# Optimization experiments

Hardware: AMD Instinct MI355X
Metric: run time of the kernel (lower is better)

The kernel has to match this reference:

```python
import jax, jax.numpy as jnp
import numpy as np

K, N, M, P, H = 8, 16, 8, 32, 32
BSZ, T = 128, 512
TAU = 0.5
P_STAY = 0.9


def setup_inputs() -> dict:
    key = jax.random.key(0)
    ks = jax.random.split(key, 20)
    f32 = jnp.float32
    norm = lambda k, s, sc=1.0: (jax.random.normal(k, s) * sc).astype(f32)
    sw = 1.0 / np.sqrt(H)  # torch GRU init scale
    return {
        "a_seq": norm(ks[0], (BSZ, T, P)),
        "A": norm(ks[1], (K, N, N), 0.1),
        "Bmat": norm(ks[2], (K, N, M), 0.1),
        "C": norm(ks[3], (K, P, N), 0.1),
        "Q": (jnp.tile(jnp.eye(N, dtype=f32)[None], (K, 1, 1)) + norm(ks[4], (K, N, N), 0.01)),
        "wih_f": norm(ks[5], (3 * H, P), sw),
        "whh_f": norm(ks[6], (3 * H, H), sw),
        "bih_f": norm(ks[7], (3 * H,), sw),
        "bhh_f": norm(ks[8], (3 * H,), sw),
        "wih_b": norm(ks[9], (3 * H, P), sw),
        "whh_b": norm(ks[10], (3 * H, H), sw),
        "bih_b": norm(ks[11], (3 * H,), sw),
        "bhh_b": norm(ks[12], (3 * H,), sw),
        "wl": norm(ks[13], (K * K, 2 * H), sw),
        "bl": norm(ks[14], (K * K,), sw),
        "wi": norm(ks[15], (K, 2 * H), sw),
        "bi": norm(ks[16], (K,), sw),
        "u0": jax.random.uniform(ks[17], (BSZ, K), minval=1e-6, maxval=1.0 - 1e-6, dtype=f32),
        "useq": jax.random.uniform(ks[18], (BSZ, T - 1, K), minval=1e-6, maxval=1.0 - 1e-6, dtype=f32),
    }


def _gru_dir(gx, whh, bhh, reverse):
    # gx: [T, B, 3H] precomputed input-to-hidden gates; torch GRU cell math
    def step(h, g):
        gh = h @ whh.T + bhh
        xr, xz, xn = jnp.split(g, 3, axis=-1)
        hr, hz, hn = jnp.split(gh, 3, axis=-1)
        r = jax.nn.sigmoid(xr + hr)
        z = jax.nn.sigmoid(xz + hz)
        n = jnp.tanh(xn + r * hn)
        h_new = (1.0 - z) * n + z * h
        return h_new, h_new
    h0 = jnp.zeros((gx.shape[1], whh.shape[1]), gx.dtype)
    _, hs = jax.lax.scan(step, h0, gx, reverse=reverse)
    return hs  # [T, B, H]


def reference(a_seq, A, Bmat, C, Q, wih_f, whh_f, bih_f, bhh_f,
              wih_b, whh_b, bih_b, bhh_b, wl, bl, wi, bi, u0, useq):
    Bn, Tn, _ = a_seq.shape
    Kn = A.shape[0]
    x = a_seq.transpose(1, 0, 2)  # [T, B, P]
    hf = _gru_dir(x @ wih_f.T + bih_f, whh_f, bhh_f, False)
    hb = _gru_dir(x @ wih_b.T + bih_b, whh_b, bhh_b, True)
    h_seq = jnp.concatenate([hf, hb], axis=-1)  # [T, B, 2H]

    logits = (h_seq @ wl.T + bl).reshape(Tn, Bn, Kn, Kn)  # [T, B, K, K]
    init_logits = h_seq[0] @ wi.T + bi                     # [B, K]

    g0 = -jnp.log(-jnp.log(u0))
    gseq = -jnp.log(-jnp.log(useq))  # [B, T-1, K]

    # t = 0 (soft gumbel-softmax since is_training=True)
    y0 = jax.nn.softmax((init_logits + g0) / TAU, axis=-1)
    lq0 = (y0 * jax.nn.log_softmax(init_logits, axis=-1)).sum(-1)
    lp0 = (y0 * jnp.log(1.0 / Kn)).sum(-1)  # torch: full_like(1/K).log()

    trans = jnp.full((Kn, Kn), (1.0 - P_STAY) / (Kn - 1), a_seq.dtype)
    trans = trans.at[jnp.arange(Kn), jnp.arange(Kn)].set(P_STAY)

    def step(y_prev, xs):
        lg, g = xs  # lg: [B, K, K], g: [B, K]
        l_t = jnp.einsum('bk,bkj->bj', y_prev, lg)
        y_t = jax.nn.softmax((l_t + g) / TAU, axis=-1)
        lq = (y_t * jax.nn.log_softmax(l_t, axis=-1)).sum(-1)
        tp = y_prev @ trans
        lp = (y_t * jnp.log(jnp.clip(tp, 1e-8))).sum(-1)
        return y_t, (y_t, lq, lp)

    _, (ys, lqs, lps) = jax.lax.scan(step, y0, (logits[1:], gseq.transpose(1, 0, 2)))

    y_seq = jnp.concatenate([y0[None], ys], axis=0).transpose(1, 0, 2)  # [B, T, K]
    log_qseq = jnp.concatenate([lq0[None], lqs], axis=0).T              # [B, T]
    log_pseq = jnp.concatenate([lp0[None], lps], axis=0).T              # [B, T]

    A_seq = jnp.einsum('btk,kij->btij', y_seq, A)
    B_seq = jnp.einsum('btk,knm->btnm', y_seq, Bmat)
    Q_seq = jnp.einsum('btk,kij->btij', y_seq, Q)
    C_seq = jnp.broadcast_to(C[0], (Bn, Tn) + C[0].shape)
    return (A_seq, B_seq, C_seq, Q_seq, log_qseq, log_pseq)
```

## Files before the change

kernel.cpp:

```cpp
#include <hip/hip_runtime.h>
#include <math.h>

#define T 512
#define B 128
#define KK 8
#define HH 32
#define PP 32

#define WS_GX    0
#define WS_GS    6291456
#define WS_HSEQ  12582912
#define WS_LOGITS 0
#define WS_INIT  16777216
#define WS_YSEQ  16778240

#define OUT_A    0
#define OUT_B    16777216
#define OUT_C    25165824
#define OUT_Q    58720256
#define OUT_LQ   75497472
#define OUT_LP   75563008

#define TINV 2.0f
#define PSTAY 0.9f
#define OFFV (0.1f / 7.0f)
#define DPS (PSTAY - OFFV)
#define LOG_INV_K (-2.0794415416798357f)

typedef float f4v __attribute__((ext_vector_type(4)));
typedef __attribute__((address_space(3))) float as3f;

__device__ __forceinline__ void dma16(unsigned ldsbyte, int voffbyte, const void* sbase) {
    asm volatile("s_mov_b32 m0, %0\n\t"
                 "global_load_lds_dwordx4 %1, %2"
                 :: "s"(ldsbyte), "v"(voffbyte), "s"(sbase)
                 : "memory");
}
__device__ __forceinline__ void st16(void* p, f4v v) {
    asm volatile("global_store_dwordx4 %0, %1, off" :: "v"(p), "v"(v) : "memory");
}
__device__ __forceinline__ f4v ldsr16(int addr) {
    f4v out;
    asm volatile("ds_read_b128 %0, %1" : "=v"(out) : "v"(addr));
    return out;
}
__device__ __forceinline__ f4v ldg16(const void* p) {
    f4v out;
    asm volatile("global_load_dwordx4 %0, %1, off" : "=v"(out) : "v"(p) : "memory");
    return out;
}
__device__ __forceinline__ float ldg4(const void* p) {
    float out;
    asm volatile("global_load_dword %0, %1, off" : "=v"(out) : "v"(p) : "memory");
    return out;
}

__global__ __launch_bounds__(192) void gx_kernel(
    const float* __restrict__ a_seq,
    const float* __restrict__ wih_f, const float* __restrict__ bih_f,
    const float* __restrict__ wih_b, const float* __restrict__ bih_b,
    float* __restrict__ gx) {
    __shared__ float xt[64 * 32];
    int blk = blockIdx.x;
    int b = blk >> 3;
    int t0 = (blk & 7) << 6;
    int g = threadIdx.x;
    int dir = (g >= 96) ? 1 : 0;
    int gg = dir ? (g - 96) : g;
    const float* w = dir ? wih_b : wih_f;
    const float* bv = dir ? bih_b : bih_f;

    {
        const float4* src = (const float4*)(a_seq + ((size_t)b * T + t0) * PP);
        float4* dst = (float4*)xt;
        for (int idx = g; idx < 512; idx += 192) dst[idx] = src[idx];
    }
    float wreg[32];
#pragma unroll
    for (int q = 0; q < 8; ++q) {
        float4 wv = *(const float4*)(w + (size_t)gg * PP + q * 4);
        wreg[q * 4 + 0] = wv.x; wreg[q * 4 + 1] = wv.y;
        wreg[q * 4 + 2] = wv.z; wreg[q * 4 + 3] = wv.w;
    }
    float bias = bv[gg];
    __syncthreads();

    float* op = gx + ((size_t)(dir * B + b) * T + t0) * 96 + gg;
#pragma unroll 4
    for (int r = 0; r < 64; ++r) {
        const float4* xr = (const float4*)(xt + r * 32);
        float acc = bias;
#pragma unroll
        for (int q = 0; q < 8; ++q) {
            float4 xv = xr[q];
            acc = fmaf(xv.x, wreg[q * 4 + 0], acc);
            acc = fmaf(xv.y, wreg[q * 4 + 1], acc);
            acc = fmaf(xv.z, wreg[q * 4 + 2], acc);
            acc = fmaf(xv.w, wreg[q * 4 + 3], acc);
        }
        op[(size_t)r * 96] = acc;
    }
}

__global__ __launch_bounds__(64, 1) void gru_kernel(
    const float* __restrict__ gx,
    const float* __restrict__ whh_f, const float* __restrict__ bhh_f,
    const float* __restrict__ whh_b, const float* __restrict__ bhh_b,
    float* __restrict__ hseq) {
    int cid = blockIdx.x;
    int b = cid & 127;
    int dir = cid >> 7;
    int i = threadIdx.x & 31;
    const float* whh = dir ? whh_b : whh_f;
    const float* bhh = dir ? bhh_b : bhh_f;
    const float* gp0 = gx + (size_t)cid * (T * 96);

    f4v wr[8], wz[8], wn[8];
#pragma unroll
    for (int q = 0; q < 8; ++q) {
        wr[q] = ldg16(whh + (size_t)i * 32 + q * 4);
        wz[q] = ldg16(whh + (size_t)(32 + i) * 32 + q * 4);
        wn[q] = ldg16(whh + (size_t)(64 + i) * 32 + q * 4);
    }
    float bhr = ldg4(bhh + i);
    float bhz = ldg4(bhh + 32 + i);
    float bhn = ldg4(bhh + 64 + i);

    const float* p = gp0 + (dir ? (T - 1) * 96 : 0);
    int gstep = dir ? -96 : 96;
    int voff = (((dir ? (T - 1) : 0) * B + b) * 64 + dir * 32 + i) * 4;
    int vstep = dir ? -(B * 64 * 4) : (B * 64 * 4);

    float pxrA[8], pxzA[8], pxnA[8], pxrB[8], pxzB[8], pxnB[8];

#define LOADG(PR, PZ, PN, G0) do {                                             \
        _Pragma("unroll")                                                      \
        for (int u_ = 0; u_ < 8; ++u_) {                                       \
            int sc_ = (G0) * 8 + u_; if (sc_ > T - 1) sc_ = T - 1;             \
            const float* rp_ = p + sc_ * gstep;                                \
            PR[u_] = ldg4(rp_ + i);                                            \
            PZ[u_] = ldg4(rp_ + 32 + i);                                       \
            PN[u_] = ldg4(rp_ + 64 + i);                                       \
        }                                                                      \
    } while (0)

#define GWAIT(N) do {                                                          \
        asm volatile("s_waitcnt vmcnt(" #N ")" ::: "memory");                  \
        __builtin_amdgcn_sched_barrier(0);                                     \
    } while (0)

#define GSTEP(PR, PZ, PN, SLOT) do {                                           \
        float hj_[32];                                                         \
        _Pragma("unroll")                                                      \
        for (int jj = 0; jj < 32; ++jj)                                        \
            hj_[jj] = __uint_as_float(                                         \
                __builtin_amdgcn_readlane(__float_as_uint(h), jj));            \
        __builtin_amdgcn_sched_barrier(0);                                     \
        float hr_ = PR[SLOT] + bhr;                                            \
        float hz_ = PZ[SLOT] + bhz;                                            \
        float hn_ = bhn;                                                       \
        _Pragma("unroll")                                                      \
        for (int q_ = 0; q_ < 8; ++q_) {                                       \
            _Pragma("unroll")                                                  \
            for (int c_ = 0; c_ < 4; ++c_) {                                   \
                float hjv_ = hj_[q_ * 4 + c_];                                 \
                hr_ = fmaf(wr[q_][c_], hjv_, hr_);                             \
                hz_ = fmaf(wz[q_][c_], hjv_, hz_);                             \
                hn_ = fmaf(wn[q_][c_], hjv_, hn_);                             \
            }                                                                  \
        }                                                                      \
        float r_ = __builtin_amdgcn_rcpf(1.f + __expf(-hr_));                  \
        float z_ = __builtin_amdgcn_rcpf(1.f + __expf(-hz_));                  \
        float na_ = fmaf(r_, hn_, PN[SLOT]);                                   \
        float e2_ = __expf(-2.f * fabsf(na_));                                 \
        float n_ = copysignf((1.f - e2_) * __builtin_amdgcn_rcpf(1.f + e2_), na_); \
        h = fmaf(z_, h - n_, n_);                                              \
        asm volatile("global_store_dword %0, %1, %2"                           \
                     :: "v"(voff), "v"(h), "s"(hseq) : "memory");              \
        voff += vstep;                                                         \
    } while (0)

    LOADG(pxrA, pxzA, pxnA, 0);
    GWAIT(0);
    float h = 0.f;

    for (int gq = 0; gq < 32; ++gq) {
        LOADG(pxrB, pxzB, pxnB, 2 * gq + 1);
        GWAIT(32);
        GSTEP(pxrA, pxzA, pxnA, 0); GSTEP(pxrA, pxzA, pxnA, 1);
        GSTEP(pxrA, pxzA, pxnA, 2); GSTEP(pxrA, pxzA, pxnA, 3);
        GSTEP(pxrA, pxzA, pxnA, 4); GSTEP(pxrA, pxzA, pxnA, 5);
        GSTEP(pxrA, pxzA, pxnA, 6); GSTEP(pxrA, pxzA, pxnA, 7);
        LOADG(pxrA, pxzA, pxnA, 2 * gq + 2);
        GWAIT(32);
        GSTEP(pxrB, pxzB, pxnB, 0); GSTEP(pxrB, pxzB, pxnB, 1);
        GSTEP(pxrB, pxzB, pxnB, 2); GSTEP(pxrB, pxzB, pxnB, 3);
        GSTEP(pxrB, pxzB, pxnB, 4); GSTEP(pxrB, pxzB, pxnB, 5);
        GSTEP(pxrB, pxzB, pxnB, 6); GSTEP(pxrB, pxzB, pxnB, 7);
    }
#undef LOADG
#undef GWAIT
#undef GSTEP
}

__global__ __launch_bounds__(256) void logits_kernel(
    const float* __restrict__ hseq,
    const float* __restrict__ wl, const float* __restrict__ bl,
    const float* __restrict__ wi, const float* __restrict__ bi,
    float* __restrict__ logits, float* __restrict__ initl) {
    __shared__ float wls[64 * 65];
    __shared__ float hrow[4][64];
    int tid = threadIdx.x;
    for (int i2 = tid; i2 < 1024; i2 += 256) {
        float4 v = ((const float4*)wl)[i2];
        int gr = i2 >> 4;
        int cc = (i2 & 15) * 4;
        float* d = &wls[gr * 65 + cc];
        d[0] = v.x; d[1] = v.y; d[2] = v.z; d[3] = v.w;
    }
    int q = tid >> 6;
    int tb = blockIdx.x * 4 + q;
    int g = tid & 63;
    hrow[q][g] = hseq[(size_t)tb * 64 + g];
    __syncthreads();
    float acc = bl[g];
    const float* wrow = &wls[g * 65];
#pragma unroll
    for (int c = 0; c < 64; ++c) acc = fmaf(wrow[c], hrow[q][c], acc);
    logits[(size_t)tb * 64 + g] = acc * TINV;
    if (tb < B && g < 8) {
        float a2 = bi[g];
        const float* w2 = wi + (size_t)g * 64;
#pragma unroll
        for (int c = 0; c < 64; ++c) a2 = fmaf(w2[c], hrow[q][c], a2);
        initl[tb * 8 + g] = a2;
    }
}

__global__ __launch_bounds__(256) void gsc_kernel(
    const float* __restrict__ u0, const float* __restrict__ useq,
    float* __restrict__ gs) {
    int id = blockIdx.x * 256 + threadIdx.x;
    if (id >= T * B * KK) return;
    int j = id & 7;
    int b = (id >> 3) & 127;
    int t = id >> 10;
    float u = (t == 0) ? u0[b * 8 + j]
                       : useq[((size_t)b * (T - 1) + (t - 1)) * 8 + j];
    gs[id] = -logf(-logf(u)) * TINV;
}

__global__ __launch_bounds__(128, 1) void scan_kernel(
    const float* __restrict__ logits, const float* __restrict__ initl,
    const float* __restrict__ gs, float* __restrict__ yseq) {
    __shared__ float lds[6][2304];
    int tid = threadIdx.x;
    int wave = tid >> 6;
    int r = tid & 63;
    int b0 = blockIdx.x * 32;
    int b = b0 + (r & 31);
    int k15 = r & 15;

    unsigned ldsU = (unsigned)(unsigned long long)(as3f*)(&lds[0][0]);

#define ISSUE(tt, sl) do {                                                   \
        unsigned lb_ = ldsU + (unsigned)((sl) * 9216);                       \
        const char* bt_ = (const char*)logits + (size_t)(tt) * 32768;        \
        const char* gt_ = (const char*)gs + (size_t)(tt) * 4096;             \
        dma16(lb_ + 0 * 1024u, lof[0], bt_);                                 \
        dma16(lb_ + 1 * 1024u, lof[1], bt_);                                 \
        dma16(lb_ + 2 * 1024u, lof[2], bt_);                                 \
        dma16(lb_ + 3 * 1024u, lof[3], bt_);                                 \
        dma16(lb_ + 4 * 1024u, lof[4], bt_);                                 \
        dma16(lb_ + 5 * 1024u, lof[5], bt_);                                 \
        dma16(lb_ + 6 * 1024u, lof[6], bt_);                                 \
        dma16(lb_ + 7 * 1024u, lof[7], bt_);                                 \
        dma16(lb_ + 8192u, gof, gt_);                                        \
    } while (0)

    if (wave == 1) {
        int lof[8];
#pragma unroll
        for (int q = 0; q < 8; ++q) {
            int rr = q * 4 + (r >> 4);
            int cc = r & 15;
            lof[q] = (((b0 + rr) * 64) + ((cc ^ (rr & 15)) << 2)) << 2;
        }
        int gof;
        {
            int rg = r >> 1;
            int cc = r & 1;
            gof = (((b0 + rg) * 8) + ((cc ^ (rg & 1)) << 2)) << 2;
        }
#pragma unroll
        for (int p = 1; p <= 5; ++p) ISSUE(p, p);
        asm volatile("s_waitcnt vmcnt(36)" ::: "memory");
        __builtin_amdgcn_s_barrier();
        for (int t = 1; t < T; ++t) {
            asm volatile("s_waitcnt vmcnt(27)" ::: "memory");
            __builtin_amdgcn_s_barrier();
            int tp = t + 5; if (tp > T - 1) tp = T - 1;
            ISSUE(tp, (t + 5) % 6);
        }
        return;
    }

    unsigned rbase = ldsU + (unsigned)((r & 31) * 256);
    unsigned gbase = ldsU + 8192u + (unsigned)((r & 31) * 32);

#define SREAD(LL, GA, GB, tt) do {                                           \
        int so_ = ((tt) % 6) * 9216;                                         \
        _Pragma("unroll")                                                    \
        for (int m_ = 0; m_ < 16; ++m_)                                      \
            LL[m_] = ldsr16((int)(rbase + so_ + ((m_ ^ k15) << 4)));         \
        GA = ldsr16((int)(gbase + so_ + ((r & 1) << 4)));                    \
        GB = ldsr16((int)(gbase + so_ + (((r & 1) ^ 1) << 4)));              \
    } while (0)

#define LWAIT() do {                                                         \
        asm volatile("s_waitcnt lgkmcnt(0)" ::: "memory");                   \
        __builtin_amdgcn_sched_barrier(0);                                   \
    } while (0)

#define SCOMP(LL, GA, GB, tt) do {                                           \
        float pl_[8];                                                        \
        _Pragma("unroll")                                                    \
        for (int j_ = 0; j_ < 8; ++j_) pl_[j_] = 0.f;                        \
        _Pragma("unroll")                                                    \
        for (int k_ = 0; k_ < 8; ++k_) {                                     \
            f4v w0_ = LL[2 * k_], w1_ = LL[2 * k_ + 1];                      \
            float ek_ = e[k_];                                               \
            pl_[0] = fmaf(ek_, w0_.x, pl_[0]); pl_[1] = fmaf(ek_, w0_.y, pl_[1]); \
            pl_[2] = fmaf(ek_, w0_.z, pl_[2]); pl_[3] = fmaf(ek_, w0_.w, pl_[3]); \
            pl_[4] = fmaf(ek_, w1_.x, pl_[4]); pl_[5] = fmaf(ek_, w1_.y, pl_[5]); \
            pl_[6] = fmaf(ek_, w1_.z, pl_[6]); pl_[7] = fmaf(ek_, w1_.w, pl_[7]); \
        }                                                                    \
        float gg_[8] = {GA.x, GA.y, GA.z, GA.w, GB.x, GB.y, GB.z, GB.w};     \
        float ss_ = 0.f;                                                     \
        _Pragma("unroll")                                                    \
        for (int j_ = 0; j_ < 8; ++j_) {                                     \
            float a_ = fmaf(pl_[j_], sinv, gg_[j_]);                         \
            e[j_] = __expf(a_);                                              \
            ss_ += e[j_];                                                    \
        }                                                                    \
        sinv = __builtin_amdgcn_rcpf(ss_);                                   \
        if (r < 32) {                                                        \
            f4v v0_ = (f4v){e[0] * sinv, e[1] * sinv, e[2] * sinv, e[3] * sinv}; \
            f4v v1_ = (f4v){e[4] * sinv, e[5] * sinv, e[6] * sinv, e[7] * sinv}; \
            st16(&yp[2 * (tt)], v0_);                                        \
            st16(&yp[2 * (tt) + 1], v1_);                                    \
        }                                                                    \
    } while (0)

    f4v* yp = (f4v*)(yseq + (size_t)b * T * 8);
    float e[8];
    float sinv;

    {
        const f4v* il4 = (const f4v*)(initl + b * 8);
        f4v i0 = il4[0], i1 = il4[1];
        const f4v* g4 = (const f4v*)(gs + b * 8);
        f4v G0 = g4[0], G1 = g4[1];
        float a[8];
        a[0] = fmaf(i0.x, TINV, G0.x); a[1] = fmaf(i0.y, TINV, G0.y);
        a[2] = fmaf(i0.z, TINV, G0.z); a[3] = fmaf(i0.w, TINV, G0.w);
        a[4] = fmaf(i1.x, TINV, G1.x); a[5] = fmaf(i1.y, TINV, G1.y);
        a[6] = fmaf(i1.z, TINV, G1.z); a[7] = fmaf(i1.w, TINV, G1.w);
        float ssum = 0.f;
#pragma unroll
        for (int j = 0; j < 8; ++j) { e[j] = __expf(a[j]); ssum += e[j]; }
        sinv = __builtin_amdgcn_rcpf(ssum);
        if (r < 32) {
            f4v y0v = (f4v){e[0] * sinv, e[1] * sinv, e[2] * sinv, e[3] * sinv};
            f4v y1v = (f4v){e[4] * sinv, e[5] * sinv, e[6] * sinv, e[7] * sinv};
            st16(&yp[0], y0v);
            st16(&yp[1], y1v);
        }
    }

    f4v LA[16], LB[16], gaA, gbA, gaB, gbB;

    __builtin_amdgcn_s_barrier();
    SREAD(LA, gaA, gbA, 1);

    for (int t = 1; t < T - 1; t += 2) {
        __builtin_amdgcn_s_barrier();
        LWAIT();
        SREAD(LB, gaB, gbB, t + 1);
        SCOMP(LA, gaA, gbA, t);

        __builtin_amdgcn_s_barrier();
        LWAIT();
        SREAD(LA, gaA, gbA, t + 2);
        SCOMP(LB, gaB, gbB, t + 1);
    }
    __builtin_amdgcn_s_barrier();
    LWAIT();
    SCOMP(LA, gaA, gbA, T - 1);
#undef ISSUE
#undef SREAD
#undef LWAIT
#undef SCOMP
}

__global__ __launch_bounds__(256) void lqlp_kernel(
    const float* __restrict__ logits, const float* __restrict__ initl,
    const float* __restrict__ yseq,
    float* __restrict__ logq, float* __restrict__ logp) {
    int tid = blockIdx.x * 256 + threadIdx.x;
    int j = tid & 7;
    int row = tid >> 3;
    int b = row >> 9;
    int t = row & (T - 1);

    const float4* yt4 = (const float4*)(yseq + (size_t)row * 8);
    float4 ya = yt4[0], yb = yt4[1];
    float yt[8] = {ya.x, ya.y, ya.z, ya.w, yb.x, yb.y, yb.z, yb.w};

    float l[8];
    float lp;
    if (t == 0) {
        const float4* il4 = (const float4*)(initl + b * 8);
        float4 i0 = il4[0], i1 = il4[1];
        l[0] = i0.x; l[1] = i0.y; l[2] = i0.z; l[3] = i0.w;
        l[4] = i1.x; l[5] = i1.y; l[6] = i1.z; l[7] = i1.w;
        float sy = ((yt[0] + yt[1]) + (yt[2] + yt[3])) + ((yt[4] + yt[5]) + (yt[6] + yt[7]));
        lp = LOG_INV_K * sy;
    } else {
        const float4* yp4 = (const float4*)(yseq + (size_t)row * 8 - 8);
        float4 p0 = yp4[0], p1 = yp4[1];
        float ypv[8] = {p0.x, p0.y, p0.z, p0.w, p1.x, p1.y, p1.z, p1.w};
        float ypj = yseq[(size_t)row * 8 - 8 + j];
        const float4* L4 = (const float4*)(logits + ((size_t)t * B + b) * 64 + j * 8);
        float4 r0 = L4[0], r1 = L4[1];
        float c[8] = {ypj * r0.x, ypj * r0.y, ypj * r0.z, ypj * r0.w,
                      ypj * r1.x, ypj * r1.y, ypj * r1.z, ypj * r1.w};
#pragma unroll
        for (int s = 1; s <= 4; s <<= 1) {
#pragma unroll
            for (int m = 0; m < 8; ++m) c[m] += __shfl_xor(c[m], s, 64);
        }
#pragma unroll
        for (int m = 0; m < 8; ++m) l[m] = c[m] * 0.5f;
        float sy = ((ypv[0] + ypv[1]) + (ypv[2] + ypv[3])) + ((ypv[4] + ypv[5]) + (ypv[6] + ypv[7]));
        float acc = 0.f;
#pragma unroll
        for (int m = 0; m < 8; ++m) {
            float tp = fmaf(DPS, ypv[m], OFFV * sy);
            acc = fmaf(yt[m], logf(fmaxf(tp, 1e-8f)), acc);
        }
        lp = acc;
    }
    float m = fmaxf(fmaxf(fmaxf(l[0], l[1]), fmaxf(l[2], l[3])),
                    fmaxf(fmaxf(l[4], l[5]), fmaxf(l[6], l[7])));
    float se = 0.f;
#pragma unroll
    for (int m2 = 0; m2 < 8; ++m2) se += __expf(l[m2] - m);
    float lse = m + logf(se);
    float lq = 0.f;
#pragma unroll
    for (int m2 = 0; m2 < 8; ++m2) lq = fmaf(yt[m2], l[m2] - lse, lq);
    if (j == 0) {
        logq[row] = lq;
        logp[row] = lp;
    }
}

__global__ __launch_bounds__(256) void out_kernel(
    const float* __restrict__ yseq,
    const float* __restrict__ A, const float* __restrict__ Bm,
    const float* __restrict__ C, const float* __restrict__ Q,
    float4* __restrict__ out4) {
    __shared__ float tab[6144];
    int tid = threadIdx.x;
    int bt0 = blockIdx.x * 64;
    {
        float4* t4 = (float4*)tab;
        const float4* A4 = (const float4*)A;
        const float4* B4 = (const float4*)Bm;
        const float4* Q4 = (const float4*)Q;
        const float4* C4 = (const float4*)C;
        for (int i2 = tid; i2 < 512; i2 += 256) t4[i2] = A4[i2];
        if (tid < 256) t4[512 + tid] = B4[tid];
        for (int i2 = tid; i2 < 512; i2 += 256) t4[768 + i2] = Q4[i2];
        if (tid < 128) t4[1280 + tid] = C4[tid];
        const float4* Y4 = (const float4*)(yseq + (size_t)bt0 * 8);
        if (tid < 128) t4[1408 + tid] = Y4[tid];
    }
    __syncthreads();

    int wave = tid >> 6;
    int lane = tid & 63;
    const float4* t4 = (const float4*)tab;

    if (wave == 0 || wave == 1) {
        int tbase = (wave == 0) ? 0 : 768;
        size_t obase = (wave == 0) ? (size_t)(OUT_A / 4) : (size_t)(OUT_Q / 4);
        float4 wreg[8];
#pragma unroll
        for (int k = 0; k < 8; ++k) wreg[k] = t4[tbase + k * 64 + lane];
        for (int bt = 0; bt < 64; ++bt) {
            float4 ya = t4[1408 + bt * 2];
            float4 yb = t4[1408 + bt * 2 + 1];
            float yk[8] = {ya.x, ya.y, ya.z, ya.w, yb.x, yb.y, yb.z, yb.w};
            float4 v = make_float4(0.f, 0.f, 0.f, 0.f);
#pragma unroll
            for (int k = 0; k < 8; ++k) {
                v.x = fmaf(yk[k], wreg[k].x, v.x);
                v.y = fmaf(yk[k], wreg[k].y, v.y);
                v.z = fmaf(yk[k], wreg[k].z, v.z);
                v.w = fmaf(yk[k], wreg[k].w, v.w);
            }
            out4[obase + (size_t)(bt0 + bt) * 64 + lane] = v;
        }
    } else if (wave == 2) {
        if (lane < 32) {
            float4 wreg[8];
#pragma unroll
            for (int k = 0; k < 8; ++k) wreg[k] = t4[512 + k * 32 + lane];
            for (int bt = 0; bt < 64; ++bt) {
                float4 ya = t4[1408 + bt * 2];
                float4 yb = t4[1408 + bt * 2 + 1];
                float yk[8] = {ya.x, ya.y, ya.z, ya.w, yb.x, yb.y, yb.z, yb.w};
                float4 v = make_float4(0.f, 0.f, 0.f, 0.f);
#pragma unroll
                for (int k = 0; k < 8; ++k) {
                    v.x = fmaf(yk[k], wreg[k].x, v.x);
                    v.y = fmaf(yk[k], wreg[k].y, v.y);
                    v.z = fmaf(yk[k], wreg[k].z, v.z);
                    v.w = fmaf(yk[k], wreg[k].w, v.w);
                }
                out4[(size_t)(OUT_B / 4) + (size_t)(bt0 + bt) * 32 + lane] = v;
            }
        } else {
            float4 c0 = t4[1280 + (lane - 32)];
            for (int bt = 0; bt < 64; ++bt)
                out4[(size_t)(OUT_C / 4) + (size_t)(bt0 + bt) * 128 + (lane - 32)] = c0;
        }
    } else {
        float4 c1 = t4[1280 + 32 + lane];
        float4 c2 = (lane < 32) ? t4[1280 + 96 + lane] : make_float4(0.f, 0.f, 0.f, 0.f);
        for (int bt = 0; bt < 64; ++bt) {
            out4[(size_t)(OUT_C / 4) + (size_t)(bt0 + bt) * 128 + 32 + lane] = c1;
            if (lane < 32)
                out4[(size_t)(OUT_C / 4) + (size_t)(bt0 + bt) * 128 + 96 + lane] = c2;
        }
    }
}

extern "C" void kernel_launch(void* const* d_in, const int* in_sizes, int n_in,
                              void* d_out, int out_size, void* d_ws, size_t ws_size,
                              hipStream_t stream) {
    const float* a_seq = (const float*)d_in[0];
    const float* A     = (const float*)d_in[1];
    const float* Bmat  = (const float*)d_in[2];
    const float* C     = (const float*)d_in[3];
    const float* Q     = (const float*)d_in[4];
    const float* wih_f = (const float*)d_in[5];
    const float* whh_f = (const float*)d_in[6];
    const float* bih_f = (const float*)d_in[7];
    const float* bhh_f = (const float*)d_in[8];
    const float* wih_b = (const float*)d_in[9];
    const float* whh_b = (const float*)d_in[10];
    const float* bih_b = (const float*)d_in[11];
    const float* bhh_b = (const float*)d_in[12];
    const float* wl    = (const float*)d_in[13];
    const float* bl    = (const float*)d_in[14];
    const float* wi    = (const float*)d_in[15];
    const float* bi    = (const float*)d_in[16];
    const float* u0    = (const float*)d_in[17];
    const float* useq  = (const float*)d_in[18];

    float* ws = (float*)d_ws;
    float* gx     = ws + WS_GX;
    float* gsb    = ws + WS_GS;
    float* hseq   = ws + WS_HSEQ;
    float* logits = ws + WS_LOGITS;
    float* initl  = ws + WS_INIT;
    float* yseq   = ws + WS_YSEQ;

    float* outf = (float*)d_out;
    float* logq = outf + OUT_LQ;
    float* logp = outf + OUT_LP;

    gx_kernel<<<B * (T / 64), 192, 0, stream>>>(a_seq, wih_f, bih_f, wih_b, bih_b, gx);
    gru_kernel<<<256, 64, 0, stream>>>(gx, whh_f, bhh_f, whh_b, bhh_b, hseq);
    {
        int total = B * T * KK;
        gsc_kernel<<<(total + 255) / 256, 256, 0, stream>>>(u0, useq, gsb);
    }
    logits_kernel<<<T * B / 4, 256, 0, stream>>>(hseq, wl, bl, wi, bi, logits, initl);
    scan_kernel<<<4, 128, 0, stream>>>(logits, initl, gsb, yseq);
    lqlp_kernel<<<B * T * KK / 256, 256, 0, stream>>>(logits, initl, yseq, logq, logp);
    out_kernel<<<B * T / 64, 256, 0, stream>>>(yseq, A, Bmat, C, Q, (float4*)d_out);
}
```

Before: 487.2 us.

## Interleave two batch chains per lane in scan kernel with shallower prefetch

Result: slower. 658.9 us (+35.2%).

```diff
diff --git a/kernel.cpp b/kernel.cpp
--- a/kernel.cpp
+++ b/kernel.cpp
@@ -253,18 +253,16 @@
 __global__ __launch_bounds__(128, 1) void scan_kernel(
     const float* __restrict__ logits, const float* __restrict__ initl,
     const float* __restrict__ gs, float* __restrict__ yseq) {
-    __shared__ float lds[6][2304];
+    __shared__ float lds[3][4608];
     int tid = threadIdx.x;
     int wave = tid >> 6;
     int r = tid & 63;
-    int b0 = blockIdx.x * 32;
-    int b = b0 + (r & 31);
-    int k15 = r & 15;
+    int b0 = blockIdx.x * 64;
 
     unsigned ldsU = (unsigned)(unsigned long long)(as3f*)(&lds[0][0]);
 
 #define ISSUE(tt, sl) do {                                                   \
-        unsigned lb_ = ldsU + (unsigned)((sl) * 9216);                       \
+        unsigned lb_ = ldsU + (unsigned)((sl) * 18432);                      \
         const char* bt_ = (const char*)logits + (size_t)(tt) * 32768;        \
         const char* gt_ = (const char*)gs + (size_t)(tt) * 4096;             \
         dma16(lb_ + 0 * 1024u, lof[0], bt_);                                 \
@@ -275,132 +273,142 @@
         dma16(lb_ + 5 * 1024u, lof[5], bt_);                                 \
         dma16(lb_ + 6 * 1024u, lof[6], bt_);                                 \
         dma16(lb_ + 7 * 1024u, lof[7], bt_);                                 \
-        dma16(lb_ + 8192u, gof, gt_);                                        \
+        dma16(lb_ + 8 * 1024u, lof[8], bt_);                                 \
+        dma16(lb_ + 9 * 1024u, lof[9], bt_);                                 \
+        dma16(lb_ + 10 * 1024u, lof[10], bt_);                               \
+        dma16(lb_ + 11 * 1024u, lof[11], bt_);                               \
+        dma16(lb_ + 12 * 1024u, lof[12], bt_);                               \
+        dma16(lb_ + 13 * 1024u, lof[13], bt_);                               \
+        dma16(lb_ + 14 * 1024u, lof[14], bt_);                               \
+        dma16(lb_ + 15 * 1024u, lof[15], bt_);                               \
+        dma16(lb_ + 16384u, gof[0], gt_);                                    \
+        dma16(lb_ + 17408u, gof[1], gt_);                                    \
     } while (0)
 
     if (wave == 1) {
-        int lof[8];
-#pragma unroll
-        for (int q = 0; q < 8; ++q) {
+        int lof[16];
+#pragma unroll
+        for (int q = 0; q < 16; ++q) {
             int rr = q * 4 + (r >> 4);
             int cc = r & 15;
             lof[q] = (((b0 + rr) * 64) + ((cc ^ (rr & 15)) << 2)) << 2;
         }
-        int gof;
-        {
-            int rg = r >> 1;
+        int gof[2];
+#pragma unroll
+        for (int d = 0; d < 2; ++d) {
+            int rg = d * 32 + (r >> 1);
             int cc = r & 1;
-            gof = (((b0 + rg) * 8) + ((cc ^ (rg & 1)) << 2)) << 2;
-        }
-#pragma unroll
-        for (int p = 1; p <= 5; ++p) ISSUE(p, p);
-        asm volatile("s_waitcnt vmcnt(36)" ::: "memory");
-        __builtin_amdgcn_s_barrier();
+            gof[d] = (((b0 + rg) * 8) + ((cc ^ (rg & 1)) << 2)) << 2;
+        }
+        ISSUE(1, 1);
+        ISSUE(2, 2);
         for (int t = 1; t < T; ++t) {
-            asm volatile("s_waitcnt vmcnt(27)" ::: "memory");
+            asm volatile("s_waitcnt vmcnt(18)" ::: "memory");
             __builtin_amdgcn_s_barrier();
-            int tp = t + 5; if (tp > T - 1) tp = T - 1;
-            ISSUE(tp, (t + 5) % 6);
+            if (t <= T - 2) {
+                int tp = t + 2; if (tp > T - 1) tp = T - 1;
+                ISSUE(tp, (t + 2) % 3);
+            }
         }
         return;
     }
 
-    unsigned rbase = ldsU + (unsigned)((r & 31) * 256);
-    unsigned gbase = ldsU + 8192u + (unsigned)((r & 31) * 32);
-
-#define SREAD(LL, GA, GB, tt) do {                                           \
-        int so_ = ((tt) % 6) * 9216;                                         \
+    int rr31 = r & 31;
+    int bA = b0 + rr31;
+    int bB = b0 + 32 + rr31;
+    int xk = rr31 & 15;
+    int gxk = rr31 & 1;
+    unsigned baseA = ldsU + (unsigned)(rr31 * 256);
+    unsigned baseB = ldsU + (unsigned)((rr31 + 32) * 256);
+    unsigned gbA = ldsU + 16384u + (unsigned)(rr31 * 32);
+    unsigned gbB = ldsU + 16384u + (unsigned)((rr31 + 32) * 32);
+
+#define SREAD(LL, G0, G1, BASE, GB) do {                                     \
         _Pragma("unroll")                                                    \
         for (int m_ = 0; m_ < 16; ++m_)                                      \
-            LL[m_] = ldsr16((int)(rbase + so_ + ((m_ ^ k15) << 4)));         \
-        GA = ldsr16((int)(gbase + so_ + ((r & 1) << 4)));                    \
-        GB = ldsr16((int)(gbase + so_ + (((r & 1) ^ 1) << 4)));              \
+            LL[m_] = ldsr16((int)(BASE + so_ + ((m_ ^ xk) << 4)));           \
+        G0 = ldsr16((int)(GB + so_ + (gxk << 4)));                           \
+        G1 = ldsr16((int)(GB + so_ + ((gxk ^ 1) << 4)));                     \
     } while (0)
 
-#define LWAIT() do {                                                         \
-        asm volatile("s_waitcnt lgkmcnt(0)" ::: "memory");                   \
-        __builtin_amdgcn_sched_barrier(0);                                   \
-    } while (0)
-
-#define SCOMP(LL, GA, GB, tt) do {                                           \
+#define SCOMP(LL, G0, G1, E, SINV, YP, tt) do {                              \
         float pl_[8];                                                        \
         _Pragma("unroll")                                                    \
         for (int j_ = 0; j_ < 8; ++j_) pl_[j_] = 0.f;                        \
         _Pragma("unroll")                                                    \
         for (int k_ = 0; k_ < 8; ++k_) {                                     \
             f4v w0_ = LL[2 * k_], w1_ = LL[2 * k_ + 1];                      \
-            float ek_ = e[k_];                                               \
+            float ek_ = E[k_];                                               \
             pl_[0] = fmaf(ek_, w0_.x, pl_[0]); pl_[1] = fmaf(ek_, w0_.y, pl_[1]); \
             pl_[2] = fmaf(ek_, w0_.z, pl_[2]); pl_[3] = fmaf(ek_, w0_.w, pl_[3]); \
             pl_[4] = fmaf(ek_, w1_.x, pl_[4]); pl_[5] = fmaf(ek_, w1_.y, pl_[5]); \
             pl_[6] = fmaf(ek_, w1_.z, pl_[6]); pl_[7] = fmaf(ek_, w1_.w, pl_[7]); \
         }                                                                    \
-        float gg_[8] = {GA.x, GA.y, GA.z, GA.w, GB.x, GB.y, GB.z, GB.w};     \
+        float gg_[8] = {G0.x, G0.y, G0.z, G0.w, G1.x, G1.y, G1.z, G1.w};     \
         float ss_ = 0.f;                                                     \
         _Pragma("unroll")                                                    \
         for (int j_ = 0; j_ < 8; ++j_) {                                     \
-            float a_ = fmaf(pl_[j_], sinv, gg_[j_]);                         \
-            e[j_] = __expf(a_);                                              \
-            ss_ += e[j_];                                                    \
+            float a_ = fmaf(pl_[j_], SINV, gg_[j_]);                         \
+            E[j_] = __expf(a_);                                              \
+            ss_ += E[j_];                                                    \
         }                                                                    \
-        sinv = __builtin_amdgcn_rcpf(ss_);                                   \
+        SINV = __builtin_amdgcn_rcpf(ss_);                                   \
         if (r < 32) {                                                        \
-            f4v v0_ = (f4v){e[0] * sinv, e[1] * sinv, e[2] * sinv, e[3] * sinv}; \
-            f4v v1_ = (f4v){e[4] * sinv, e[5] * sinv, e[6] * sinv, e[7] * sinv}; \
-            st16(&yp[2 * (tt)], v0_);                                        \
-            st16(&yp[2 * (tt) + 1], v1_);                                    \
+            f4v v0_ = (f4v){E[0] * SINV, E[1] * SINV, E[2] * SINV, E[3] * SINV}; \
+            f4v v1_ = (f4v){E[4] * SINV, E[5] * SINV, E[6] * SINV, E[7] * SINV}; \
+            st16(&YP[2 * (tt)], v0_);                                        \
+            st16(&YP[2 * (tt) + 1], v1_);                                    \
         }                                                                    \
     } while (0)
 
-    f4v* yp = (f4v*)(yseq + (size_t)b * T * 8);
-    float e[8];
-    float sinv;
-
-    {
-        const f4v* il4 = (const f4v*)(initl + b * 8);
-        f4v i0 = il4[0], i1 = il4[1];
-        const f4v* g4 = (const f4v*)(gs + b * 8);
-        f4v G0 = g4[0], G1 = g4[1];
-        float a[8];
-        a[0] = fmaf(i0.x, TINV, G0.x); a[1] = fmaf(i0.y, TINV, G0.y);
-        a[2] = fmaf(i0.z, TINV, G0.z); a[3] = fmaf(i0.w, TINV, G0.w);
-        a[4] = fmaf(i1.x, TINV, G1.x); a[5] = fmaf(i1.y, TINV, G1.y);
-        a[6] = fmaf(i1.z, TINV, G1.z); a[7] = fmaf(i1.w, TINV, G1.w);
-        float ssum = 0.f;
-#pragma unroll
-        for (int j = 0; j < 8; ++j) { e[j] = __expf(a[j]); ssum += e[j]; }
-        sinv = __builtin_amdgcn_rcpf(ssum);
-        if (r < 32) {
-            f4v y0v = (f4v){e[0] * sinv, e[1] * sinv, e[2] * sinv, e[3] * sinv};
-            f4v y1v = (f4v){e[4] * sinv, e[5] * sinv, e[6] * sinv, e[7] * sinv};
-            st16(&yp[0], y0v);
-            st16(&yp[1], y1v);
-        }
-    }
-
-    f4v LA[16], LB[16], gaA, gbA, gaB, gbB;
-
-    __builtin_amdgcn_s_barrier();
-    SREAD(LA, gaA, gbA, 1);
-
-    for (int t = 1; t < T - 1; t += 2) {
+#define T0INIT(BG, E, SINV, YP) do {                                         \
+        const f4v* il4_ = (const f4v*)(initl + (BG) * 8);                    \
+        f4v i0_ = il4_[0], i1_ = il4_[1];                                    \
+        const f4v* g4_ = (const f4v*)(gs + (BG) * 8);                        \
+        f4v G0_ = g4_[0], G1_ = g4_[1];                                      \
+        float a_[8];                                                         \
+        a_[0] = fmaf(i0_.x, TINV, G0_.x); a_[1] = fmaf(i0_.y, TINV, G0_.y);  \
+        a_[2] = fmaf(i0_.z, TINV, G0_.z); a_[3] = fmaf(i0_.w, TINV, G0_.w);  \
+        a_[4] = fmaf(i1_.x, TINV, G1_.x); a_[5] = fmaf(i1_.y, TINV, G1_.y);  \
+        a_[6] = fmaf(i1_.z, TINV, G1_.z); a_[7] = fmaf(i1_.w, TINV, G1_.w);  \
+        float ss_ = 0.f;                                                     \
+        _Pragma("unroll")                                                    \
+        for (int j_ = 0; j_ < 8; ++j_) { E[j_] = __expf(a_[j_]); ss_ += E[j_]; } \
+        SINV = __builtin_amdgcn_rcpf(ss_);                                   \
+        if (r < 32) {                                                        \
+            f4v y0_ = (f4v){E[0] * SINV, E[1] * SINV, E[2] * SINV, E[3] * SINV}; \
+            f4v y1_ = (f4v){E[4] * SINV, E[5] * SINV, E[6] * SINV, E[7] * SINV}; \
+            st16(&YP[0], y0_);                                               \
+            st16(&YP[1], y1_);                                               \
+        }                                                                    \
+    } while (0)
+
+    f4v* ypA = (f4v*)(yseq + (size_t)bA * T * 8);
+    f4v* ypB = (f4v*)(yseq + (size_t)bB * T * 8);
+    float eA[8], eB[8];
+    float sinvA, sinvB;
+
+    T0INIT(bA, eA, sinvA, ypA);
+    T0INIT(bB, eB, sinvB, ypB);
+
+    f4v LA[16], LB[16], gaA, gbAv, gaB, gbBv;
+
+    for (int t = 1; t < T; ++t) {
         __builtin_amdgcn_s_barrier();
-        LWAIT();
-        SREAD(LB, gaB, gbB, t + 1);
-        SCOMP(LA, gaA, gbA, t);
-
-        __builtin_amdgcn_s_barrier();
-        LWAIT();
-        SREAD(LA, gaA, gbA, t + 2);
-        SCOMP(LB, gaB, gbB, t + 1);
-    }
-    __builtin_amdgcn_s_barrier();
-    LWAIT();
-    SCOMP(LA, gaA, gbA, T - 1);
+        int so_ = (t % 3) * 18432;
+        SREAD(LA, gaA, gbAv, baseA, gbA);
+        SREAD(LB, gaB, gbBv, baseB, gbB);
+        asm volatile("s_waitcnt lgkmcnt(15)" ::: "memory");
+        __builtin_amdgcn_sched_barrier(0);
+        SCOMP(LA, gaA, gbAv, eA, sinvA, ypA, t);
+        asm volatile("s_waitcnt lgkmcnt(0)" ::: "memory");
+        __builtin_amdgcn_sched_barrier(0);
+        SCOMP(LB, gaB, gbBv, eB, sinvB, ypB, t);
+    }
 #undef ISSUE
 #undef SREAD
-#undef LWAIT
 #undef SCOMP
+#undef T0INIT
 }
 
 __global__ __launch_bounds__(256) void lqlp_kernel(
@@ -590,7 +598,7 @@
         gsc_kernel<<<(total + 255) / 256, 256, 0, stream>>>(u0, useq, gsb);
     }
     logits_kernel<<<T * B / 4, 256, 0, stream>>>(hseq, wl, bl, wi, bi, logits, initl);
-    scan_kernel<<<4, 128, 0, stream>>>(logits, initl, gsb, yseq);
+    scan_kernel<<<2, 128, 0, stream>>>(logits, initl, gsb, yseq);
     lqlp_kernel<<<B * T * KK / 256, 256, 0, stream>>>(logits, initl, yseq, logq, logp);
     out_kernel<<<B * T / 64, 256, 0, stream>>>(yseq, A, Bmat, C, Q, (float4*)d_out);
 }
```
